# Kernel tuning notes

Hardware: AMD Instinct MI355X
Metric: run time of the kernel (lower is better)

The kernel has to match this reference:

```python
import jax, jax.numpy as jnp
import numpy as np

HIDDEN = 2048
N_HEADS = 16
HEAD_DIM = HIDDEN // N_HEADS  # 128
EPS = 1e-6
ROPE_BASE = 10000.0


def _rope_cos_sin(position_ids):
    # position_ids: [B, S] int -> cos/sin [B, S, HEAD_DIM//2] (neox half-split style)
    inv_freq = 1.0 / (ROPE_BASE ** (jnp.arange(0, HEAD_DIM, 2, dtype=jnp.float32) / HEAD_DIM))
    angles = position_ids.astype(jnp.float32)[..., None] * inv_freq  # [B,S,D/2]
    return jnp.cos(angles), jnp.sin(angles)


def _apply_rope(x, cos, sin):
    # x: [B, S, H, D]; cos/sin: [B, S, 1, D/2]
    d2 = HEAD_DIM // 2
    x1, x2 = x[..., :d2], x[..., d2:]
    return jnp.concatenate([x1 * cos - x2 * sin, x2 * cos + x1 * sin], axis=-1)


def _rmsnorm(x, w):
    # normalize over last dim (head_dim) in fp32, as in IdeficsRMSNorm
    xf = x.astype(jnp.float32)
    var = jnp.mean(xf * xf, axis=-1, keepdims=True)
    return (w * (xf * jax.lax.rsqrt(var + EPS))).astype(x.dtype)


def setup_inputs() -> dict:
    key = jax.random.key(0)
    k1, k2, k3, k4 = jax.random.split(key, 4)
    B, S = 2, 2048
    hidden_states = jax.random.normal(k1, (B, S, HIDDEN), dtype=jnp.float32)
    w_qkv = jax.random.normal(k2, (3 * HIDDEN, HIDDEN), dtype=jnp.float32) * (HIDDEN ** -0.5)
    w_o = jax.random.normal(k3, (HIDDEN, HIDDEN), dtype=jnp.float32) * (HIDDEN ** -0.5)
    q_ln_w = jnp.ones((HEAD_DIM,), dtype=jnp.float32)
    k_ln_w = jnp.ones((HEAD_DIM,), dtype=jnp.float32)
    position_ids = jnp.sort(jax.random.randint(k4, (B, S), 0, S), axis=-1).astype(jnp.int64)
    return {"hidden_states": hidden_states, "w_qkv": w_qkv, "w_o": w_o,
            "q_ln_w": q_ln_w, "k_ln_w": k_ln_w, "position_ids": position_ids}


def reference(hidden_states, w_qkv, w_o, q_ln_w, k_ln_w, position_ids):
    B, S, _ = hidden_states.shape
    # fused QKV projection (Linear: x @ W^T, no bias)
    qkv = jnp.einsum('bsh,oh->bso', hidden_states, w_qkv)  # [B,S,3*HIDDEN]
    q, k, v = jnp.split(qkv, 3, axis=-1)
    q = q.reshape(B, S, N_HEADS, HEAD_DIM)
    k = k.reshape(B, S, N_HEADS, HEAD_DIM)
    v = v.reshape(B, S, N_HEADS, HEAD_DIM)
    # rotary embedding
    cos, sin = _rope_cos_sin(position_ids)
    cos, sin = cos[:, :, None, :], sin[:, :, None, :]  # [B,S,1,D/2]
    q = _apply_rope(q, cos, sin)
    k = _apply_rope(k, cos, sin)
    # optional per-head QK RMSNorm
    q = _rmsnorm(q, q_ln_w)
    k = _rmsnorm(k, k_ln_w)
    # SDPA (no mask, dropout=0), scale = 1/sqrt(head_dim)
    scale = HEAD_DIM ** -0.5
    scores = jnp.einsum('bqhd,bkhd->bhqk', q, k) * scale
    probs = jax.nn.softmax(scores, axis=-1)
    attn = jnp.einsum('bhqk,bkhd->bqhd', probs, v)  # [B,S,H,D]
    attn = attn.reshape(B, S, HIDDEN)
    return jnp.einsum('bsh,oh->bso', attn, w_o)
```

## Files before the change

### kernel.cpp

```cpp
#include <hip/hip_runtime.h>
#include <math.h>

#define S_   2048
#define H_   2048
#define NH_  16
#define HD_  128
#define M_   4096
#define TH_  6144

typedef __attribute__((ext_vector_type(8))) short bf16x8;
typedef __attribute__((ext_vector_type(4))) float f32x4;

__device__ __forceinline__ ushort f2bf(float x) {
  unsigned u = __float_as_uint(x);
  u = (u + 0x7FFFu + ((u >> 16) & 1u)) >> 16;
  return (ushort)u;
}

__device__ __forceinline__ void gll16(const void* g, void* l) {
  __builtin_amdgcn_global_load_lds(
      (const __attribute__((address_space(1))) void*)g,
      (__attribute__((address_space(3))) void*)l, 16, 0, 0);
}

__global__ void cvt_kernel(const float* __restrict__ src,
                           ushort* __restrict__ dst, int n4) {
  int i = blockIdx.x * blockDim.x + threadIdx.x;
  if (i < n4) {
    float4 v = ((const float4*)src)[i];
    ushort4 o;
    o.x = f2bf(v.x); o.y = f2bf(v.y); o.z = f2bf(v.z); o.w = f2bf(v.w);
    ((ushort4*)dst)[i] = o;
  }
}

__global__ void rope_tab(const int* __restrict__ pos,
                         float* __restrict__ ct, float* __restrict__ st) {
  int idx = blockIdx.x * blockDim.x + threadIdx.x;
  int m = idx >> 6, d = idx & 63;
  float invf = exp2f(-(float)d * 0.20762050593046020f);
  float ang = (float)pos[m] * invf;
  float s, c;
  sincosf(ang, &s, &c);
  ct[idx] = c;
  st[idx] = s;
}

template <int EPI>
__global__ __launch_bounds__(256, 2) void gemm_bt(
    const ushort* __restrict__ A, const ushort* __restrict__ Bm,
    float* __restrict__ C, int Ndim, int Kdim,
    const float* __restrict__ qln, const float* __restrict__ kln,
    const float* __restrict__ ct, const float* __restrict__ st,
    ushort* __restrict__ qbuf, ushort* __restrict__ kbuf,
    ushort* __restrict__ vt)
{
  __shared__ ushort As[128 * 32];
  __shared__ ushort Bs[128 * 32];
  const int t = threadIdx.x, l = t & 63, w = t >> 6;
  const int q4 = l >> 4, c0 = l & 15;
  const int m0 = blockIdx.y * 128, n0 = blockIdx.x * 128;

  const ushort* ga0 = A  + (size_t)(m0 + 32 * w + (l >> 2)) * Kdim + (l & 3) * 8;
  const ushort* ga1 = ga0 + (size_t)16 * Kdim;
  const ushort* gb0 = Bm + (size_t)(n0 + 32 * w + (l >> 2)) * Kdim + (l & 3) * 8;
  const ushort* gb1 = gb0 + (size_t)16 * Kdim;
  ushort* lA0 = As + (32 * w) * 32;
  ushort* lA1 = As + (32 * w + 16) * 32;
  ushort* lB0 = Bs + (32 * w) * 32;
  ushort* lB1 = Bs + (32 * w + 16) * 32;

  f32x4 acc[2][8];
#pragma unroll
  for (int i = 0; i < 2; ++i)
#pragma unroll
    for (int j = 0; j < 8; ++j) acc[i][j] = (f32x4){0.f, 0.f, 0.f, 0.f};

  for (int k0 = 0; k0 < Kdim; k0 += 32) {
    gll16(ga0 + k0, lA0);
    gll16(ga1 + k0, lA1);
    gll16(gb0 + k0, lB0);
    gll16(gb1 + k0, lB1);
    __syncthreads();
    bf16x8 af[2], bfr[8];
#pragma unroll
    for (int i = 0; i < 2; ++i)
      af[i] = *(const bf16x8*)(As + (32 * w + 16 * i + c0) * 32 + q4 * 8);
#pragma unroll
    for (int j = 0; j < 8; ++j)
      bfr[j] = *(const bf16x8*)(Bs + (16 * j + c0) * 32 + q4 * 8);
#pragma unroll
    for (int i = 0; i < 2; ++i)
#pragma unroll
      for (int j = 0; j < 8; ++j)
        acc[i][j] = __builtin_amdgcn_mfma_f32_16x16x32_bf16(
            af[i], bfr[j], acc[i][j], 0, 0, 0);
    __syncthreads();
  }

  if (EPI == 0) {
#pragma unroll
    for (int i = 0; i < 2; ++i)
#pragma unroll
      for (int j = 0; j < 8; ++j) {
        float* cp = C + (size_t)(m0 + 32 * w + 16 * i + q4 * 4) * Ndim
                      + n0 + 16 * j + c0;
#pragma unroll
        for (int r = 0; r < 4; ++r) cp[(size_t)r * Ndim] = acc[i][j][r];
      }
  } else {
    const int seg = blockIdx.x >> 4;
    const int h = blockIdx.x & 15;
    if (seg < 2) {
      const float* lnw = (seg == 0) ? qln : kln;
      ushort* obuf = (seg == 0) ? qbuf : kbuf;
      float wl[8];
#pragma unroll
      for (int j = 0; j < 8; ++j) wl[j] = lnw[16 * j + c0];
#pragma unroll
      for (int i = 0; i < 2; ++i)
#pragma unroll
        for (int r = 0; r < 4; ++r) {
          const int m = m0 + 32 * w + 16 * i + q4 * 4 + r;
          const int b = m >> 11, s = m & 2047;
          float y[8], ss = 0.f;
#pragma unroll
          for (int j = 0; j < 4; ++j) {
            const int d = 16 * j + c0;
            const float cs = ct[m * 64 + d], sn = st[m * 64 + d];
            const float x1 = acc[i][j][r], x2 = acc[i][j + 4][r];
            y[j]     = x1 * cs - x2 * sn;
            y[j + 4] = x2 * cs + x1 * sn;
          }
#pragma unroll
          for (int j = 0; j < 8; ++j) ss += y[j] * y[j];
          ss += __shfl_xor(ss, 1, 16);
          ss += __shfl_xor(ss, 2, 16);
          ss += __shfl_xor(ss, 4, 16);
          ss += __shfl_xor(ss, 8, 16);
          const float sc = rsqrtf(ss * (1.f / 128.f) + 1e-6f);
          ushort* dst = obuf + ((size_t)(b * NH_ + h) * S_ + s) * HD_;
#pragma unroll
          for (int j = 0; j < 8; ++j) dst[16 * j + c0] = f2bf(y[j] * wl[j] * sc);
        }
    } else {
      const int b = m0 >> 11;
      const int s0 = (m0 & 2047) + 32 * w + q4 * 4;
#pragma unroll
      for (int i = 0; i < 2; ++i)
#pragma unroll
        for (int j = 0; j < 8; ++j) {
          const int d = 16 * j + c0;
          const int s = s0 + 16 * i;
          ushort4 o;
          o.x = f2bf(acc[i][j][0]); o.y = f2bf(acc[i][j][1]);
          o.z = f2bf(acc[i][j][2]); o.w = f2bf(acc[i][j][3]);
          *(ushort4*)(vt + ((size_t)(b * NH_ + h) * HD_ + d) * S_ + s) = o;
        }
    }
  }
}

__global__ __launch_bounds__(256, 2) void attn_mfma(
    const ushort* __restrict__ qb, const ushort* __restrict__ kb,
    const ushort* __restrict__ vtb, ushort* __restrict__ ob)
{
  __shared__ ushort Ks[64 * 128];
  __shared__ ushort Vs[128 * 64];
  __shared__ ushort Ps[128 * 64];
  const int t = threadIdx.x, l = t & 63, w = t >> 6;
  const int q4 = l >> 4, c0 = l & 15;
  const int q0 = blockIdx.x * 128, h = blockIdx.y, b = blockIdx.z;
  const ushort* qh = qb + (size_t)(b * NH_ + h) * S_ * HD_;
  const ushort* kh = kb + (size_t)(b * NH_ + h) * S_ * HD_;
  const ushort* vh = vtb + (size_t)(b * NH_ + h) * HD_ * S_;

  bf16x8 qf[2][4];
#pragma unroll
  for (int i = 0; i < 2; ++i)
#pragma unroll
    for (int kc = 0; kc < 4; ++kc)
      qf[i][kc] = *(const bf16x8*)(qh + (size_t)(q0 + 32 * w + 16 * i + c0) * HD_
                                   + kc * 32 + q4 * 8);

  f32x4 Of[2][8];
#pragma unroll
  for (int i = 0; i < 2; ++i)
#pragma unroll
    for (int j = 0; j < 8; ++j) Of[i][j] = (f32x4){0.f, 0.f, 0.f, 0.f};
  float lI[8];
#pragma unroll
  for (int i = 0; i < 8; ++i) lI[i] = 0.f;

  const float scale = 0.08838834764831843f;

  for (int kv0 = 0; kv0 < S_; kv0 += 64) {
    __syncthreads();
#pragma unroll
    for (int j2 = 0; j2 < 4; ++j2) {
      {
        const int rowK = 16 * w + 4 * j2 + q4;
        gll16(kh + (size_t)(kv0 + rowK) * HD_ + (c0 ^ (rowK & 7)) * 8,
              Ks + (16 * w + 4 * j2) * 128);
      }
      {
        const int rowV = 32 * w + 8 * j2 + (l >> 3);
        gll16(vh + (size_t)rowV * S_ + kv0 + (((l & 7) ^ (rowV & 7)) * 8),
              Vs + (32 * w + 8 * j2) * 64);
      }
    }
    __syncthreads();

    f32x4 Sv[2][4];
#pragma unroll
    for (int i = 0; i < 2; ++i)
#pragma unroll
      for (int j = 0; j < 4; ++j) Sv[i][j] = (f32x4){0.f, 0.f, 0.f, 0.f};
#pragma unroll
    for (int kc = 0; kc < 4; ++kc) {
      bf16x8 kf[4];
#pragma unroll
      for (int j = 0; j < 4; ++j) {
        const int row = 16 * j + c0;
        kf[j] = *(const bf16x8*)(Ks + row * 128 + (((kc * 4 + q4) ^ (row & 7)) * 8));
      }
#pragma unroll
      for (int i = 0; i < 2; ++i)
#pragma unroll
        for (int j = 0; j < 4; ++j)
          Sv[i][j] = __builtin_amdgcn_mfma_f32_16x16x32_bf16(
              qf[i][kc], kf[j], Sv[i][j], 0, 0, 0);
    }

#pragma unroll
    for (int i = 0; i < 2; ++i)
#pragma unroll
      for (int r = 0; r < 4; ++r) {
        const int idx = i * 4 + r;
        const float p0 = __expf(__builtin_fmaf(Sv[i][0][r], scale, -12.0f));
        const float p1 = __expf(__builtin_fmaf(Sv[i][1][r], scale, -12.0f));
        const float p2 = __expf(__builtin_fmaf(Sv[i][2][r], scale, -12.0f));
        const float p3 = __expf(__builtin_fmaf(Sv[i][3][r], scale, -12.0f));
        lI[idx] += (p0 + p1) + (p2 + p3);
        const int qrow = 32 * w + 16 * i + q4 * 4 + r;
        const int x = qrow & 7, cb = c0 & 7, ch = c0 >> 3;
        Ps[qrow * 64 + ((0 + ch) ^ x) * 8 + cb] = f2bf(p0);
        Ps[qrow * 64 + ((2 + ch) ^ x) * 8 + cb] = f2bf(p1);
        Ps[qrow * 64 + ((4 + ch) ^ x) * 8 + cb] = f2bf(p2);
        Ps[qrow * 64 + ((6 + ch) ^ x) * 8 + cb] = f2bf(p3);
      }

#pragma unroll
    for (int kc2 = 0; kc2 < 2; ++kc2) {
      bf16x8 pa[2];
#pragma unroll
      for (int i = 0; i < 2; ++i) {
        const int row = 32 * w + 16 * i + c0;
        pa[i] = *(const bf16x8*)(Ps + row * 64 + (((kc2 * 4 + q4) ^ (row & 7)) * 8));
      }
#pragma unroll
      for (int jd = 0; jd < 8; ++jd) {
        const int row = 16 * jd + c0;
        const bf16x8 vf =
            *(const bf16x8*)(Vs + row * 64 + (((kc2 * 4 + q4) ^ (row & 7)) * 8));
#pragma unroll
        for (int i = 0; i < 2; ++i)
          Of[i][jd] = __builtin_amdgcn_mfma_f32_16x16x32_bf16(
              pa[i], vf, Of[i][jd], 0, 0, 0);
      }
    }
  }

#pragma unroll
  for (int idx = 0; idx < 8; ++idx) {
    lI[idx] += __shfl_xor(lI[idx], 1, 16);
    lI[idx] += __shfl_xor(lI[idx], 2, 16);
    lI[idx] += __shfl_xor(lI[idx], 4, 16);
    lI[idx] += __shfl_xor(lI[idx], 8, 16);
  }

#pragma unroll
  for (int i = 0; i < 2; ++i)
#pragma unroll
    for (int r = 0; r < 4; ++r) {
      const int q = q0 + 32 * w + 16 * i + q4 * 4 + r;
      const float inv = 1.f / lI[i * 4 + r];
      ushort* dst = ob + ((size_t)b * S_ + q) * H_ + h * HD_;
#pragma unroll
      for (int jd = 0; jd < 8; ++jd)
        dst[16 * jd + c0] = f2bf(Of[i][jd][r] * inv);
    }
}

extern "C" void kernel_launch(void* const* d_in, const int* in_sizes, int n_in,
                              void* d_out, int out_size, void* d_ws, size_t ws_size,
                              hipStream_t stream)
{
  const float* hs   = (const float*)d_in[0];
  const float* wqkv = (const float*)d_in[1];
  const float* wo   = (const float*)d_in[2];
  const float* qln  = (const float*)d_in[3];
  const float* kln  = (const float*)d_in[4];
  const int*   pos  = (const int*)d_in[5];

  ushort* ws    = (ushort*)d_ws;
  ushort* hsb   = ws;
  ushort* wqkvb = hsb + 8388608;
  ushort* wob   = wqkvb + 12582912;
  ushort* qbuf  = wob + 4194304;
  ushort* kbuf  = qbuf + 8388608;
  ushort* vt    = kbuf + 8388608;
  ushort* atb   = vt + 8388608;
  float*  ct    = (float*)(atb + 8388608);
  float*  st    = ct + 262144;

  cvt_kernel<<<8192, 256, 0, stream>>>(hs, hsb, 2097152);
  cvt_kernel<<<12288, 256, 0, stream>>>(wqkv, wqkvb, 3145728);
  cvt_kernel<<<4096, 256, 0, stream>>>(wo, wob, 1048576);
  rope_tab<<<1024, 256, 0, stream>>>(pos, ct, st);

  gemm_bt<1><<<dim3(TH_ / 128, M_ / 128), 256, 0, stream>>>(
      hsb, wqkvb, nullptr, TH_, H_, qln, kln, ct, st, qbuf, kbuf, vt);

  attn_mfma<<<dim3(S_ / 128, NH_, 2), 256, 0, stream>>>(qbuf, kbuf, vt, atb);

  gemm_bt<0><<<dim3(H_ / 128, M_ / 128), 256, 0, stream>>>(
      atb, wob, (float*)d_out, H_, H_, nullptr, nullptr, nullptr, nullptr,
      nullptr, nullptr, nullptr);
}
```

Baseline: 422.7 us.

## Double-buffer K/V tiles in LDS to overlap loads with attention compute

The attention kernel now keeps two LDS buffers for the K and V tiles. It issues the asynchronous global-to-LDS load for the next KV block before computing on the current one, and needs only one barrier per tile instead of two. The goal is to hide global load latency behind the MFMA and softmax work. In exchange, LDS use per block rises from about 48KB to 80KB, which still allows the two blocks per CU requested by the launch bounds but leaves no headroom for more.

```diff
diff --git a/kernel.cpp b/kernel.cpp
--- a/kernel.cpp
+++ b/kernel.cpp
@@ -165,8 +165,8 @@
     const ushort* __restrict__ qb, const ushort* __restrict__ kb,
     const ushort* __restrict__ vtb, ushort* __restrict__ ob)
 {
-  __shared__ ushort Ks[64 * 128];
-  __shared__ ushort Vs[128 * 64];
+  __shared__ ushort Ks[2][64 * 128];
+  __shared__ ushort Vs[2][128 * 64];
   __shared__ ushort Ps[128 * 64];
   const int t = threadIdx.x, l = t & 63, w = t >> 6;
   const int q4 = l >> 4, c0 = l & 15;
@@ -194,23 +194,19 @@
 
   const float scale = 0.08838834764831843f;
 
-  for (int kv0 = 0; kv0 < S_; kv0 += 64) {
-    __syncthreads();
+  auto STAGE = [&](int buf, int kv0) {
 #pragma unroll
     for (int j2 = 0; j2 < 4; ++j2) {
-      {
-        const int rowK = 16 * w + 4 * j2 + q4;
-        gll16(kh + (size_t)(kv0 + rowK) * HD_ + (c0 ^ (rowK & 7)) * 8,
-              Ks + (16 * w + 4 * j2) * 128);
-      }
-      {
-        const int rowV = 32 * w + 8 * j2 + (l >> 3);
-        gll16(vh + (size_t)rowV * S_ + kv0 + (((l & 7) ^ (rowV & 7)) * 8),
-              Vs + (32 * w + 8 * j2) * 64);
-      }
-    }
-    __syncthreads();
-
+      const int rowK = 16 * w + 4 * j2 + q4;
+      gll16(kh + (size_t)(kv0 + rowK) * HD_ + (c0 ^ (rowK & 7)) * 8,
+            &Ks[buf][(16 * w + 4 * j2) * 128]);
+      const int rowV = 32 * w + 8 * j2 + (l >> 3);
+      gll16(vh + (size_t)rowV * S_ + kv0 + (((l & 7) ^ (rowV & 7)) * 8),
+            &Vs[buf][(32 * w + 8 * j2) * 64]);
+    }
+  };
+
+  auto COMPUTE = [&](int buf) {
     f32x4 Sv[2][4];
 #pragma unroll
     for (int i = 0; i < 2; ++i)
@@ -222,7 +218,8 @@
 #pragma unroll
       for (int j = 0; j < 4; ++j) {
         const int row = 16 * j + c0;
-        kf[j] = *(const bf16x8*)(Ks + row * 128 + (((kc * 4 + q4) ^ (row & 7)) * 8));
+        kf[j] = *(const bf16x8*)(&Ks[buf][row * 128 +
+                                          (((kc * 4 + q4) ^ (row & 7)) * 8)]);
       }
 #pragma unroll
       for (int i = 0; i < 2; ++i)
@@ -256,19 +253,32 @@
 #pragma unroll
       for (int i = 0; i < 2; ++i) {
         const int row = 32 * w + 16 * i + c0;
-        pa[i] = *(const bf16x8*)(Ps + row * 64 + (((kc2 * 4 + q4) ^ (row & 7)) * 8));
+        pa[i] = *(const bf16x8*)(Ps + row * 64 +
+                                 (((kc2 * 4 + q4) ^ (row & 7)) * 8));
       }
 #pragma unroll
       for (int jd = 0; jd < 8; ++jd) {
         const int row = 16 * jd + c0;
-        const bf16x8 vf =
-            *(const bf16x8*)(Vs + row * 64 + (((kc2 * 4 + q4) ^ (row & 7)) * 8));
+        const bf16x8 vf = *(const bf16x8*)(&Vs[buf][row * 64 +
+                                   (((kc2 * 4 + q4) ^ (row & 7)) * 8)]);
 #pragma unroll
         for (int i = 0; i < 2; ++i)
           Of[i][jd] = __builtin_amdgcn_mfma_f32_16x16x32_bf16(
               pa[i], vf, Of[i][jd], 0, 0, 0);
       }
     }
+  };
+
+  STAGE(0, 0);
+  __syncthreads();
+
+  for (int it = 0; it < S_ / 64; it += 2) {
+    STAGE(1, (it + 1) * 64);
+    COMPUTE(0);
+    __syncthreads();
+    if (it + 2 < S_ / 64) STAGE(0, (it + 2) * 64);
+    COMPUTE(1);
+    __syncthreads();
   }
 
 #pragma unroll
```

After: 411.7 us. 1.03x faster.
